# Optimization experiments

Hardware: AMD Instinct MI355X
Metric: run time of the kernel (lower is better)

## Reference

```python
import jax, jax.numpy as jnp
import numpy as np

IMAGE_SHAPE = (3, 256, 256)
IMAGE_SIZE = int(np.prod(IMAGE_SHAPE))  # 196608
N_BATCH = 8
N_SEG_P1 = 33  # n_segments + 1


def setup_inputs() -> dict:
    key = jax.random.key(0)
    k1, k2 = jax.random.split(key)
    segment_x = jax.random.uniform(k1, (N_BATCH, N_SEG_P1), dtype=jnp.float32)
    segment_y = jax.random.uniform(k2, (N_BATCH, N_SEG_P1), dtype=jnp.float32)
    return {"segment_x": segment_x, "segment_y": segment_y}


def _fix_x_order(segment_x, segment_y):
    # The torch loop repeatedly copies x[i] over x[i+1] when x[i] > x[i+1];
    # its fixed point is the running max of x along the segment axis, with y
    # carried from the position achieving that max (ties keep the later entry).
    def combine(a, b):
        xa, ya = a
        xb, yb = b
        take_b = xb >= xa
        return jnp.where(take_b, xb, xa), jnp.where(take_b, yb, ya)

    return jax.lax.associative_scan(combine, (segment_x, segment_y), axis=1)


def reference(segment_x, segment_y):
    # x_in: normalized pixel coordinates in (0, 1], shape [S, 1, 1]
    x_in = (jnp.arange(1, IMAGE_SIZE + 1, dtype=jnp.float32) / IMAGE_SIZE)[:, None, None]
    x, y = _fix_x_order(segment_x, segment_y)  # [B, N+1] each, x non-decreasing

    # mask: [S, B, N] one-hot-ish segment membership
    lt = x_in < x[:, 1:]
    ge = x_in >= x[:, :-1]
    mask = lt & ge
    first = mask[:, :, :1] | (x_in < x[:, :1])    # clamp below first knot
    last = mask[:, :, -1:] | (x_in >= x[:, -1:])  # clamp above last knot
    mask = jnp.concatenate([first, mask[:, :, 1:-1], last], axis=2)

    divider = x[:, 1:] - x[:, :-1]
    divider = jnp.where(divider == 0.0, 0.0001, divider)
    ratio = (y[:, 1:] - y[:, :-1]) / divider  # [B, N]

    m = mask.astype(x.dtype)
    ypred = (ratio * m * (x_in - x[:, :-1]) + m * y[:, :-1]).sum(axis=2)  # [S, B]
    return ypred.T  # [B, S]
```

## Files before the change

### kernel.cpp

```cpp
#include <hip/hip_runtime.h>


constexpr int S = 196608;
constexpr int NSEG = 32;
constexpr int ELEMS_PER_THREAD = 4;
constexpr int BLOCK = 256;
constexpr int ELEMS_PER_BLOCK = BLOCK * ELEMS_PER_THREAD;

__global__ __launch_bounds__(BLOCK) void decoder_kernel(
    const float* __restrict__ seg_x,
    const float* __restrict__ seg_y,
    float* __restrict__ out)
{
    __shared__ float xs[NSEG + 1];
    __shared__ float ys[NSEG + 1];
    __shared__ float ratio[NSEG];

    const int b = blockIdx.y;
    const int tid = threadIdx.x;

    if (tid == 0) {
        const float* px = seg_x + b * (NSEG + 1);
        const float* py = seg_y + b * (NSEG + 1);
        float cx = px[0];
        float cy = py[0];
        xs[0] = cx; ys[0] = cy;
        for (int i = 1; i <= NSEG; ++i) {
            float xi = px[i];
            float yi = py[i];
            if (xi >= cx) { cx = xi; cy = yi; }
            xs[i] = cx; ys[i] = cy;
        }
    }
    __syncthreads();

    if (tid < NSEG) {
        float d = xs[tid + 1] - xs[tid];
        if (d == 0.0f) d = 0.0001f;
        ratio[tid] = (ys[tid + 1] - ys[tid]) / d;
    }
    __syncthreads();

    const int s_base = blockIdx.x * ELEMS_PER_BLOCK + tid * ELEMS_PER_THREAD;

    float4 res;
    float* rp = &res.x;
#pragma unroll
    for (int e = 0; e < ELEMS_PER_THREAD; ++e) {
        const int s = s_base + e;
        const float xin = (float)(s + 1) / (float)S;

        int j = 0;
#pragma unroll
        for (int k = 1; k < NSEG; ++k) {
            j += (xin >= xs[k]) ? 1 : 0;
        }
        rp[e] = fmaf(ratio[j], xin - xs[j], ys[j]);
    }

    *reinterpret_cast<float4*>(&out[(size_t)b * S + s_base]) = res;
}

extern "C" void kernel_launch(void* const* d_in, const int* in_sizes, int n_in,
                              void* d_out, int out_size, void* d_ws, size_t ws_size,
                              hipStream_t stream) {
    const float* seg_x = (const float*)d_in[0];
    const float* seg_y = (const float*)d_in[1];
    float* out = (float*)d_out;

    dim3 grid(S / ELEMS_PER_BLOCK, 8);
    decoder_kernel<<<grid, BLOCK, 0, stream>>>(seg_x, seg_y, out);
}
```

Before: 62.03 us.

## Parallelize knot prefix-max with wave shuffles and double per-thread work

Result: faster. 60.57 us (-2.4%).

```diff
diff --git a/kernel.cpp b/kernel.cpp
--- a/kernel.cpp
+++ b/kernel.cpp
@@ -2,63 +2,72 @@
 
 
 constexpr int S = 196608;
+constexpr int NK = 33;
 constexpr int NSEG = 32;
-constexpr int ELEMS_PER_THREAD = 4;
 constexpr int BLOCK = 256;
-constexpr int ELEMS_PER_BLOCK = BLOCK * ELEMS_PER_THREAD;
+constexpr int EPT = 8;
+constexpr int EPB = BLOCK * EPT;
+constexpr int HALF = BLOCK * 4;
 
 __global__ __launch_bounds__(BLOCK) void decoder_kernel(
     const float* __restrict__ seg_x,
     const float* __restrict__ seg_y,
     float* __restrict__ out)
 {
-    __shared__ float xs[NSEG + 1];
-    __shared__ float ys[NSEG + 1];
+    __shared__ float xs[NK];
+    __shared__ float ys[NK];
     __shared__ float ratio[NSEG];
 
     const int b = blockIdx.y;
     const int tid = threadIdx.x;
 
-    if (tid == 0) {
-        const float* px = seg_x + b * (NSEG + 1);
-        const float* py = seg_y + b * (NSEG + 1);
-        float cx = px[0];
-        float cy = py[0];
-        xs[0] = cx; ys[0] = cy;
-        for (int i = 1; i <= NSEG; ++i) {
-            float xi = px[i];
-            float yi = py[i];
-            if (xi >= cx) { cx = xi; cy = yi; }
-            xs[i] = cx; ys[i] = cy;
+    if (tid < 64) {
+        float x = 0.0f, y = 0.0f;
+        if (tid < NK) {
+            x = seg_x[b * NK + tid];
+            y = seg_y[b * NK + tid];
+        }
+#pragma unroll
+        for (int d = 1; d < 64; d <<= 1) {
+            float ox = __shfl_up(x, d);
+            float oy = __shfl_up(y, d);
+            if (tid >= d && x < ox) { x = ox; y = oy; }
+        }
+        float xn = __shfl_down(x, 1);
+        float yn = __shfl_down(y, 1);
+        if (tid < NK) { xs[tid] = x; ys[tid] = y; }
+        if (tid < NSEG) {
+            float dx = xn - x;
+            if (dx == 0.0f) dx = 0.0001f;
+            ratio[tid] = (yn - y) / dx;
         }
     }
     __syncthreads();
 
-    if (tid < NSEG) {
-        float d = xs[tid + 1] - xs[tid];
-        if (d == 0.0f) d = 0.0001f;
-        ratio[tid] = (ys[tid + 1] - ys[tid]) / d;
+    float xr[NSEG];
+#pragma unroll
+    for (int k = 0; k < NSEG; ++k) xr[k] = xs[k];
+
+    const size_t obase = (size_t)b * S;
+
+#pragma unroll
+    for (int h = 0; h < 2; ++h) {
+        const int s0 = blockIdx.x * EPB + h * HALF + tid * 4;
+        float tmp[4];
+#pragma unroll
+        for (int e = 0; e < 4; ++e) {
+            const float xin = (float)(s0 + e + 1) / (float)S;
+            int j = 0;
+#pragma unroll
+            for (int k = 1; k < NSEG; ++k) {
+                j += (xin >= xr[k]) ? 1 : 0;
+            }
+            tmp[e] = fmaf(ratio[j], xin - xs[j], ys[j]);
+        }
+        float4 v;
+        v.x = tmp[0]; v.y = tmp[1]; v.z = tmp[2]; v.w = tmp[3];
+        *reinterpret_cast<float4*>(&out[obase + s0]) = v;
     }
-    __syncthreads();
-
-    const int s_base = blockIdx.x * ELEMS_PER_BLOCK + tid * ELEMS_PER_THREAD;
-
-    float4 res;
-    float* rp = &res.x;
-#pragma unroll
-    for (int e = 0; e < ELEMS_PER_THREAD; ++e) {
-        const int s = s_base + e;
-        const float xin = (float)(s + 1) / (float)S;
-
-        int j = 0;
-#pragma unroll
-        for (int k = 1; k < NSEG; ++k) {
-            j += (xin >= xs[k]) ? 1 : 0;
-        }
-        rp[e] = fmaf(ratio[j], xin - xs[j], ys[j]);
-    }
-
-    *reinterpret_cast<float4*>(&out[(size_t)b * S + s_base]) = res;
 }
 
 extern "C" void kernel_launch(void* const* d_in, const int* in_sizes, int n_in,
@@ -68,6 +77,6 @@
     const float* seg_y = (const float*)d_in[1];
     float* out = (float*)d_out;
 
-    dim3 grid(S / ELEMS_PER_BLOCK, 8);
+    dim3 grid(S / EPB, 8);
     decoder_kernel<<<grid, BLOCK, 0, stream>>>(seg_x, seg_y, out);
 }
```
